# Kernel tuning notes

Hardware: AMD Instinct MI355X
Metric: run time of the kernel (lower is better)

## Reference

```python
import jax, jax.numpy as jnp
import numpy as np
from jax import lax

N, G, L, D, E, STEPS = 65536, 128, 512, 128, 262144, 6
C = 2 * D  # concat dim (input_dim + output_dim)


def setup_inputs() -> dict:
    key = jax.random.key(0)
    ks = jax.random.split(key, 12)
    sD = 1.0 / float(np.sqrt(D))
    sC = 1.0 / float(np.sqrt(C))
    return {
        "x": jax.random.normal(ks[0], (N, D), jnp.float32),
        "edge_index": jax.random.randint(ks[1], (2, E), 0, N, dtype=jnp.int32),
        "edge_weight": jax.random.uniform(ks[2], (E,), jnp.float32),
        "batch": (jnp.arange(N) // L).astype(jnp.int32),  # sorted graph ids, L nodes/graph
        "ggnn_w": jax.random.normal(ks[3], (STEPS, D, D), jnp.float32) * sD,
        "gru_wih": jax.random.normal(ks[4], (3 * D, D), jnp.float32) * sD,
        "gru_whh": jax.random.normal(ks[5], (3 * D, D), jnp.float32) * sD,
        "gru_bih": jnp.zeros((3 * D,), jnp.float32),
        "gru_bhh": jnp.zeros((3 * D,), jnp.float32),
        "conv1_w": jax.random.normal(ks[6], (D, D, 3), jnp.float32) * sD,
        "conv1_b": jnp.zeros((D,), jnp.float32),
        "conv2_w": jax.random.normal(ks[7], (D, D, 1), jnp.float32) * sD,
        "conv2_b": jnp.zeros((D,), jnp.float32),
        "convc1_w": jax.random.normal(ks[8], (C, C, 3), jnp.float32) * sC,
        "convc1_b": jnp.zeros((C,), jnp.float32),
        "convc2_w": jax.random.normal(ks[9], (C, C, 1), jnp.float32) * sC,
        "convc2_b": jnp.zeros((C,), jnp.float32),
        "bn1_g": jnp.ones((D,), jnp.float32),
        "bn1_b": jnp.zeros((D,), jnp.float32),
        "bn2_g": jnp.ones((C,), jnp.float32),
        "bn2_b": jnp.zeros((C,), jnp.float32),
        "mlpy_w": jax.random.normal(ks[10], (2, D), jnp.float32) * sD,
        "mlpy_b": jnp.zeros((2,), jnp.float32),
        "mlpz_w": jax.random.normal(ks[11], (2, C), jnp.float32) * sC,
        "mlpz_b": jnp.zeros((2,), jnp.float32),
    }


def _gru(m, h, wih, whh, bih, bhh):
    gx = m @ wih.T + bih
    gh = h @ whh.T + bhh
    xr, xz, xn = jnp.split(gx, 3, axis=-1)
    hr, hz, hn = jnp.split(gh, 3, axis=-1)
    r = jax.nn.sigmoid(xr + hr)
    z = jax.nn.sigmoid(xz + hz)
    n = jnp.tanh(xn + r * hn)
    return (1.0 - z) * n + z * h


def _conv1d(x, w, b):  # x [G,Cin,L], w [Cout,Cin,K]
    y = lax.conv_general_dilated(x, w, (1,), "VALID", dimension_numbers=("NCH", "OIH", "NCH"))
    return y + b[None, :, None]


def _maxpool(x, k, s):
    return lax.reduce_window(x, -jnp.inf, lax.max, (1, 1, k), (1, 1, s), "VALID")


def _bn(x, g, b):  # training-mode BatchNorm1d over (N, L) per channel
    mean = x.mean(axis=(0, 2), keepdims=True)
    var = x.var(axis=(0, 2), keepdims=True)
    return (x - mean) * lax.rsqrt(var + 1e-5) * g[None, :, None] + b[None, :, None]


def reference(x, edge_index, edge_weight, batch, ggnn_w, gru_wih, gru_whh, gru_bih,
              gru_bhh, conv1_w, conv1_b, conv2_w, conv2_b, convc1_w, convc1_b,
              convc2_w, convc2_b, bn1_g, bn1_b, bn2_g, bn2_b, mlpy_w, mlpy_b,
              mlpz_w, mlpz_b):
    src, dst = edge_index[0], edge_index[1]

    # GatedGraphConv: per layer linear -> weighted message scatter-add -> GRU update
    def step(h, w):
        m = h @ w
        agg = jax.ops.segment_sum(m[src] * edge_weight[:, None], dst, num_segments=N)
        return _gru(agg, h, gru_wih, gru_whh, gru_bih, gru_bhh), None

    h, _ = lax.scan(step, x, ggnn_w)

    # de_batchify_graphs: one fused scatter into zero-padded [G, L, *] tensor
    counts = jax.ops.segment_sum(jnp.ones((N,), jnp.int32), batch, num_segments=G)
    offsets = jnp.cumsum(counts) - counts
    pos = jnp.arange(N) - offsets[batch]
    x_i = jnp.zeros((G, L, D), x.dtype).at[batch, pos].set(x)
    h_i = jnp.zeros((G, L, D), h.dtype).at[batch, pos].set(h)
    c_i = jnp.concatenate([h_i, x_i], axis=-1)  # [G, L, 2D]

    hT = h_i.transpose(0, 2, 1)  # [G, D, L]
    Y1 = _maxpool(jax.nn.relu(_bn(_conv1d(hT, conv1_w, conv1_b), bn1_g, bn1_b)), 3, 2)
    Y2 = _maxpool(jax.nn.relu(_bn(_conv1d(Y1, conv2_w, conv2_b), bn1_g, bn1_b)), 2, 2).transpose(0, 2, 1)
    cT = c_i.transpose(0, 2, 1)  # [G, 2D, L]
    Z1 = _maxpool(jax.nn.relu(_bn(_conv1d(cT, convc1_w, convc1_b), bn2_g, bn2_b)), 3, 2)
    Z2 = _maxpool(jax.nn.relu(_bn(_conv1d(Z1, convc2_w, convc2_b), bn2_g, bn2_b)), 2, 2).transpose(0, 2, 1)

    before_avg = (Y2 @ mlpy_w.T + mlpy_b) * (Z2 @ mlpz_w.T + mlpz_b)  # [G, L', 2]
    return before_avg.mean(axis=1)  # [G, 2]
```

## Files before the change

### kernel.cpp

```cpp
#include <hip/hip_runtime.h>
#include <math.h>

#define NN 65536
#define GG 128
#define LL 512
#define DD 128
#define EE 262144
#define NSTEPS 6
#define CC 256
#define L1 510
#define P1 254
#define P2 127

typedef __attribute__((ext_vector_type(8))) short s8bf;
typedef __attribute__((ext_vector_type(4))) float f4acc;

__device__ __forceinline__ unsigned short f2bf(float x) {
  unsigned u = __float_as_uint(x);
  unsigned r = u + 0x7FFFu + ((u >> 16) & 1u);
  return (unsigned short)(r >> 16);
}
__device__ __forceinline__ float bf2f(unsigned short h) {
  return __uint_as_float(((unsigned)h) << 16);
}
__device__ __forceinline__ unsigned short f2bf_sel(float x, int lo_sel) {
  unsigned short hi = f2bf(x);
  if (!lo_sel) return hi;
  return f2bf(x - bf2f(hi));
}
__device__ __forceinline__ uint2 pack4bf(float4 v, int lo_sel) {
  unsigned short s0 = f2bf_sel(v.x, lo_sel), s1 = f2bf_sel(v.y, lo_sel);
  unsigned short s2 = f2bf_sel(v.z, lo_sel), s3 = f2bf_sel(v.w, lo_sel);
  uint2 pk; pk.x = (unsigned)s0 | ((unsigned)s1 << 16);
  pk.y = (unsigned)s2 | ((unsigned)s3 << 16);
  return pk;
}

__global__ __launch_bounds__(256) void k_prep(
    const float* __restrict__ wih, const float* __restrict__ whh,
    const float* __restrict__ gw,
    const float* __restrict__ w1, const float* __restrict__ wc1,
    const float* __restrict__ w2, const float* __restrict__ wc2,
    unsigned short* __restrict__ whhCh, unsigned short* __restrict__ whhCl,
    unsigned short* __restrict__ c1h, unsigned short* __restrict__ c1l,
    unsigned short* __restrict__ cc1h, unsigned short* __restrict__ cc1l,
    unsigned short* __restrict__ c2h, unsigned short* __restrict__ c2l,
    unsigned short* __restrict__ cc2h, unsigned short* __restrict__ cc2l) {
  int i = blockIdx.x * 256 + threadIdx.x;
  if (i < 49152) {
    float u = whh[i];
    unsigned short h2 = f2bf(u);
    whhCh[i] = h2; whhCl[i] = f2bf(u - bf2f(h2));
  }
  if (i < 49152) {
    int ci = i & 127; int r = i >> 7; int co = r & 127; int tap = r >> 7;
    float v = w1[(co * 128 + ci) * 3 + tap];
    unsigned short h_ = f2bf(v);
    c1h[i] = h_; c1l[i] = f2bf(v - bf2f(h_));
  }
  if (i < 196608) {
    int ci = i & 255; int r = i >> 8; int co = r & 255; int tap = r >> 8;
    float v = wc1[(co * 256 + ci) * 3 + tap];
    unsigned short h_ = f2bf(v);
    cc1h[i] = h_; cc1l[i] = f2bf(v - bf2f(h_));
  }
  if (i < 16384) {
    float v = w2[i];
    unsigned short h_ = f2bf(v);
    c2h[i] = h_; c2l[i] = f2bf(v - bf2f(h_));
  }
  if (i < 65536) {
    float v = wc2[i];
    unsigned short h_ = f2bf(v);
    cc2h[i] = h_; cc2l[i] = f2bf(v - bf2f(h_));
  }
}

__global__ __launch_bounds__(256) void k_combine(
    const float* __restrict__ gw, const float* __restrict__ wih,
    unsigned short* __restrict__ WcH, unsigned short* __restrict__ WcL) {
  int i = blockIdx.x * 256 + threadIdx.x;
  int s = i / 49152;
  int r = i % 49152;
  int d = r >> 7, k = r & 127;
  const float4* ga = (const float4*)&gw[(s << 14) + k * 128];
  const float4* wa = (const float4*)&wih[d * 128];
  float4 av = make_float4(0.f, 0.f, 0.f, 0.f);
#pragma unroll 8
  for (int c = 0; c < 32; c++) {
    float4 g4 = ga[c], w4 = wa[c];
    av.x += g4.x * w4.x; av.y += g4.y * w4.y;
    av.z += g4.z * w4.z; av.w += g4.w * w4.w;
  }
  float acc = (av.x + av.y) + (av.z + av.w);
  unsigned short h_ = f2bf(acc);
  WcH[i] = h_;
  WcL[i] = f2bf(acc - bf2f(h_));
}

__global__ __launch_bounds__(256) void k_castx(const float* __restrict__ x,
                                               unsigned short* __restrict__ xH,
                                               unsigned short* __restrict__ xL) {
  int i = blockIdx.x * 256 + threadIdx.x;
  const float4* x4 = (const float4*)x;
  float4 a = x4[i * 2 + 0];
  float4 b = x4[i * 2 + 1];
  uint2 ha = pack4bf(a, 0), hb = pack4bf(b, 0);
  uint2 la = pack4bf(a, 1), lb = pack4bf(b, 1);
  uint4 hv; hv.x = ha.x; hv.y = ha.y; hv.z = hb.x; hv.w = hb.y;
  uint4 lv; lv.x = la.x; lv.y = la.y; lv.z = lb.x; lv.w = lb.y;
  *(uint4*)&xH[i * 8] = hv;
  *(uint4*)&xL[i * 8] = lv;
}

__global__ __launch_bounds__(256) void k_hist(const int* __restrict__ dst, int* __restrict__ cnt) {
  int e = blockIdx.x * 256 + threadIdx.x;
  if (e < EE) atomicAdd(&cnt[dst[e]], 1);
}

__global__ __launch_bounds__(1024) void k_scan(const int* __restrict__ cnt,
                                               int* __restrict__ rowptr,
                                               int* __restrict__ cursor) {
  __shared__ int part[1024];
  int t = threadIdx.x;
  int base = t * 64;
  int s = 0;
  for (int i = 0; i < 64; i++) s += cnt[base + i];
  part[t] = s;
  __syncthreads();
  for (int off = 1; off < 1024; off <<= 1) {
    int v = part[t];
    int u = (t >= off) ? part[t - off] : 0;
    __syncthreads();
    part[t] = v + u;
    __syncthreads();
  }
  int run = part[t] - s;
  for (int i = 0; i < 64; i++) {
    rowptr[base + i] = run;
    cursor[base + i] = run;
    run += cnt[base + i];
  }
  if (t == 1023) rowptr[NN] = run;
}

__global__ __launch_bounds__(256) void k_fill(const int* __restrict__ src,
                                              const int* __restrict__ dst,
                                              const float* __restrict__ ew,
                                              int* __restrict__ cursor,
                                              int* __restrict__ col,
                                              float* __restrict__ wgt) {
  int e = blockIdx.x * 256 + threadIdx.x;
  if (e < EE) {
    int d = dst[e];
    int p = atomicAdd(&cursor[d], 1);
    col[p] = src[e];
    wgt[p] = ew[e];
  }
}

__global__ __launch_bounds__(256) void k_gather(
    const unsigned short* __restrict__ hH, const unsigned short* __restrict__ hL,
    const int* __restrict__ rowptr, const int* __restrict__ col,
    const float* __restrict__ wgt,
    unsigned short* __restrict__ aggH, unsigned short* __restrict__ aggL) {
  int t = threadIdx.x;
  int n = blockIdx.x * 8 + (t >> 5);
  int cb = (t & 31) * 4;
  int s0 = rowptr[n], s1 = rowptr[n + 1];
  float ax = 0.f, ay = 0.f, az = 0.f, aw = 0.f;
  int e = s0;
  for (; e + 2 <= s1; e += 2) {
    int cA = col[e], cB = col[e + 1];
    float wA = wgt[e], wB = wgt[e + 1];
    uint2 hA = *(const uint2*)&hH[cA * 128 + cb];
    uint2 lA = *(const uint2*)&hL[cA * 128 + cb];
    uint2 hB = *(const uint2*)&hH[cB * 128 + cb];
    uint2 lB = *(const uint2*)&hL[cB * 128 + cb];
    float a0 = __uint_as_float(hA.x << 16) + __uint_as_float(lA.x << 16);
    float a1 = __uint_as_float(hA.x & 0xFFFF0000u) + __uint_as_float(lA.x & 0xFFFF0000u);
    float a2 = __uint_as_float(hA.y << 16) + __uint_as_float(lA.y << 16);
    float a3 = __uint_as_float(hA.y & 0xFFFF0000u) + __uint_as_float(lA.y & 0xFFFF0000u);
    float b0 = __uint_as_float(hB.x << 16) + __uint_as_float(lB.x << 16);
    float b1 = __uint_as_float(hB.x & 0xFFFF0000u) + __uint_as_float(lB.x & 0xFFFF0000u);
    float b2 = __uint_as_float(hB.y << 16) + __uint_as_float(lB.y << 16);
    float b3 = __uint_as_float(hB.y & 0xFFFF0000u) + __uint_as_float(lB.y & 0xFFFF0000u);
    ax += a0 * wA + b0 * wB;
    ay += a1 * wA + b1 * wB;
    az += a2 * wA + b2 * wB;
    aw += a3 * wA + b3 * wB;
  }
  if (e < s1) {
    int cA = col[e];
    float wA = wgt[e];
    uint2 hA = *(const uint2*)&hH[cA * 128 + cb];
    uint2 lA = *(const uint2*)&hL[cA * 128 + cb];
    float a0 = __uint_as_float(hA.x << 16) + __uint_as_float(lA.x << 16);
    float a1 = __uint_as_float(hA.x & 0xFFFF0000u) + __uint_as_float(lA.x & 0xFFFF0000u);
    float a2 = __uint_as_float(hA.y << 16) + __uint_as_float(lA.y << 16);
    float a3 = __uint_as_float(hA.y & 0xFFFF0000u) + __uint_as_float(lA.y & 0xFFFF0000u);
    ax += a0 * wA; ay += a1 * wA; az += a2 * wA; aw += a3 * wA;
  }
  unsigned short h0 = f2bf(ax), h1 = f2bf(ay), h2 = f2bf(az), h3 = f2bf(aw);
  unsigned short l0 = f2bf(ax - bf2f(h0)), l1 = f2bf(ay - bf2f(h1));
  unsigned short l2 = f2bf(az - bf2f(h2)), l3 = f2bf(aw - bf2f(h3));
  uint2 hpk, lpk;
  hpk.x = (unsigned)h0 | ((unsigned)h1 << 16); hpk.y = (unsigned)h2 | ((unsigned)h3 << 16);
  lpk.x = (unsigned)l0 | ((unsigned)l1 << 16); lpk.y = (unsigned)l2 | ((unsigned)l3 << 16);
  int base = n * 128 + cb;
  *(uint2*)&aggH[base] = hpk;
  *(uint2*)&aggL[base] = lpk;
}

__global__ __launch_bounds__(256, 2) void k_gru_mfma(
    const unsigned short* __restrict__ aggH, const unsigned short* __restrict__ aggL,
    const unsigned short* __restrict__ hinH, const unsigned short* __restrict__ hinL,
    const unsigned short* __restrict__ wxh, const unsigned short* __restrict__ wxl,
    const unsigned short* __restrict__ whhCh, const unsigned short* __restrict__ whhCl,
    const float* __restrict__ bih, const float* __restrict__ bhh,
    unsigned short* __restrict__ houtH, unsigned short* __restrict__ houtL) {
  __shared__ __attribute__((aligned(16))) unsigned short As[2 * 64 * 136];
  int t = threadIdx.x;
  int r0 = blockIdx.x * 64;
  int d0 = blockIdx.y * 64;
  int wv = t >> 6, lane = t & 63;
  int ln = lane & 15, q = lane >> 4;
  f4acc acc[4][6];
#pragma unroll
  for (int mt = 0; mt < 4; mt++)
#pragma unroll
    for (int tg = 0; tg < 6; tg++) acc[mt][tg] = (f4acc)0.f;

  for (int p = 0; p < 3; p++) {
    if (p != 1) {
      const unsigned short* s0 = (p == 2) ? aggL : aggH;
      const unsigned short* s1 = (p == 2) ? hinL : hinH;
      if (p) __syncthreads();
#pragma unroll
      for (int it = 0; it < 8; it++) {
        int v8 = it * 256 + t;
        int mat = v8 >> 10;
        int row = (v8 >> 4) & 63, k = (v8 & 15) * 8;
        const unsigned short* S = mat ? s1 : s0;
        *(uint4*)&As[mat * 8704 + row * 136 + k] = *(const uint4*)&S[(r0 + row) * 128 + k];
      }
      __syncthreads();
    }
    const unsigned short* wx = (p == 1) ? wxl : wxh;
    const unsigned short* wh = (p == 1) ? whhCl : whhCh;
#pragma unroll
    for (int k0 = 0; k0 < 128; k0 += 32) {
      s8bf af[2][4], bfr[6];
#pragma unroll
      for (int tg = 0; tg < 6; tg++) {
        int gate = (tg < 3) ? tg : tg - 3;
        const unsigned short* W = (tg < 3) ? wx : wh;
        bfr[tg] = *(const s8bf*)&W[(gate * 128 + d0 + wv * 16 + ln) * 128 + k0 + q * 8];
      }
#pragma unroll
      for (int mat = 0; mat < 2; mat++)
#pragma unroll
        for (int mt = 0; mt < 4; mt++)
          af[mat][mt] = *(const s8bf*)&As[mat * 8704 + (mt * 16 + ln) * 136 + k0 + q * 8];
#pragma unroll
      for (int mt = 0; mt < 4; mt++)
#pragma unroll
        for (int tg = 0; tg < 6; tg++)
          acc[mt][tg] = __builtin_amdgcn_mfma_f32_16x16x32_bf16(
              af[tg < 3 ? 0 : 1][mt], bfr[tg], acc[mt][tg], 0, 0, 0);
    }
  }
  int d = d0 + wv * 16 + ln;
  float bi0 = bih[d], bi1 = bih[128 + d], bi2 = bih[256 + d];
  float bh0 = bhh[d], bh1 = bhh[128 + d], bh2 = bhh[256 + d];
#pragma unroll
  for (int mt = 0; mt < 4; mt++) {
#pragma unroll
    for (int reg = 0; reg < 4; reg++) {
      int r = r0 + mt * 16 + q * 4 + reg;
      int idx = r * 128 + d;
      float hold = bf2f(hinH[idx]) + bf2f(hinL[idx]);
      float xr = acc[mt][0][reg] + bi0;
      float xz = acc[mt][1][reg] + bi1;
      float xn = acc[mt][2][reg] + bi2;
      float hr = acc[mt][3][reg] + bh0;
      float hz = acc[mt][4][reg] + bh1;
      float hn = acc[mt][5][reg] + bh2;
      float rr = 1.f / (1.f + expf(-(xr + hr)));
      float zz = 1.f / (1.f + expf(-(xz + hz)));
      float nnv = tanhf(xn + rr * hn);
      float hv = (1.f - zz) * nnv + zz * hold;
      unsigned short hh = f2bf(hv);
      houtH[idx] = hh;
      houtL[idx] = f2bf(hv - bf2f(hh));
    }
  }
}

template<int CIN, int TAPS, int WA>
__global__ __launch_bounds__(256, 4) void k_conv_mfma(
    const unsigned short* __restrict__ hiA, const unsigned short* __restrict__ hiB,
    const unsigned short* __restrict__ loA, const unsigned short* __restrict__ loB,
    const unsigned short* __restrict__ Wh, const unsigned short* __restrict__ Wl,
    const float* __restrict__ bias, float* __restrict__ out,
    float* __restrict__ stats, int Lin, int Lco) {
  constexpr int APAD = CIN + 8;
  constexpr int ROWS = 64 + TAPS - 1;
  constexpr int NCH = CIN / 32;
  constexpr int TOT8 = ROWS * CIN / 8;
  constexpr int NIT = (TOT8 + 255) / 256;
  constexpr int NINNER = TAPS * NCH;
  __shared__ __attribute__((aligned(16))) unsigned short As[ROWS * APAD];
  __shared__ float sred[256];
  const int g = blockIdx.z, co0 = blockIdx.y * 128, l0 = blockIdx.x * 64;
  const int t = threadIdx.x;
  const int wv = t >> 6, lane = t & 63, ln = lane & 15, q = lane >> 4;
  f4acc acc[4][2];
#pragma unroll
  for (int mt = 0; mt < 4; mt++)
#pragma unroll
    for (int nt = 0; nt < 2; nt++) acc[mt][nt] = (f4acc)0.f;

  for (int p = 0; p < 3; p++) {
    if (p != 1) {
      const unsigned short* pA = (p == 2) ? loA : hiA;
      const unsigned short* pB = (p == 2) ? loB : hiB;
      if (p) __syncthreads();
#pragma unroll
      for (int it = 0; it < NIT; it++) {
        int v8 = it * 256 + t;
        if (NIT * 256 == TOT8 || v8 < TOT8) {
          int row = (v8 * 8) / CIN, ch = (v8 * 8) % CIN;
          int lr = l0 + row; if (lr > Lin - 1) lr = Lin - 1;
          uint4 v;
          if (ch < WA) v = *(const uint4*)&pA[(g * Lin + lr) * WA + ch];
          else         v = *(const uint4*)&pB[(g * Lin + lr) * WA + ch - WA];
          *(uint4*)&As[row * APAD + ch] = v;
        }
      }
      __syncthreads();
    }
    const unsigned short* W = (p == 1) ? Wl : Wh;
    s8bf bcur[2], bnxt[2];
#pragma unroll
    for (int nt = 0; nt < 2; nt++)
      bcur[nt] = *(const s8bf*)&W[(co0 + wv * 32 + nt * 16 + ln) * CIN + q * 8];
#pragma unroll
    for (int it = 0; it < NINNER; it++) {
      const int tap = it / NCH, ch = it % NCH;
      if (it + 1 < NINNER) {
        const int ntap = (it + 1) / NCH, nch = (it + 1) % NCH;
#pragma unroll
        for (int nt = 0; nt < 2; nt++)
          bnxt[nt] = *(const s8bf*)&W[(ntap * CIN + co0 + wv * 32 + nt * 16 + ln) * CIN + nch * 32 + q * 8];
      }
      const int c0 = ch * 32;
      s8bf af[4];
#pragma unroll
      for (int mt = 0; mt < 4; mt++)
        af[mt] = *(const s8bf*)&As[(mt * 16 + ln + tap) * APAD + c0 + q * 8];
#pragma unroll
      for (int mt = 0; mt < 4; mt++)
#pragma unroll
        for (int nt = 0; nt < 2; nt++)
          acc[mt][nt] = __builtin_amdgcn_mfma_f32_16x16x32_bf16(af[mt], bcur[nt], acc[mt][nt], 0, 0, 0);
      if (it + 1 < NINNER) { bcur[0] = bnxt[0]; bcur[1] = bnxt[1]; }
    }
  }
  sred[t] = 0.f;
  __syncthreads();
#pragma unroll
  for (int nt = 0; nt < 2; nt++) {
    int cl = wv * 32 + nt * 16 + ln;
    int co = co0 + cl;
    float bv = bias[co];
    float s = 0.f, s2 = 0.f;
#pragma unroll
    for (int mt = 0; mt < 4; mt++)
#pragma unroll
      for (int reg = 0; reg < 4; reg++) {
        int l = l0 + mt * 16 + q * 4 + reg;
        if (l < Lco) {
          float v = acc[mt][nt][reg] + bv;
          out[(g * Lco + l) * CIN + co] = v;
          s += v; s2 += v * v;
        }
      }
    atomicAdd(&sred[cl], s);
    atomicAdd(&sred[128 + cl], s2);
  }
  __syncthreads();
  if (t < 128) atomicAdd(&stats[co0 + t], sred[t]);
  else atomicAdd(&stats[CIN + co0 + (t - 128)], sred[t]);
}

template<bool PLANES>
__global__ __launch_bounds__(256) void k_bnpool(const float* __restrict__ in,
                                                float* __restrict__ outF,
                                                unsigned short* __restrict__ outH,
                                                unsigned short* __restrict__ outL,
                                                const float* __restrict__ stats,
                                                const float* __restrict__ gamma,
                                                const float* __restrict__ beta,
                                                int Cch, int LinC, int Lout, int pk) {
  int idx = blockIdx.x * 256 + threadIdx.x;
  int total = GG * Cch * Lout;
  if (idx >= total) return;
  int c = idx & (Cch - 1);
  int r = idx / Cch;
  int p = r % Lout;
  int g = r / Lout;
  float cntf = (float)(GG * LinC);
  float mean = stats[c] / cntf;
  float var = stats[Cch + c] / cntf - mean * mean;
  float inv = rsqrtf(var + 1e-5f) * gamma[c];
  float sh = beta[c] - mean * inv;
  const float* base = &in[((g * LinC) + 2 * p) * Cch + c];
  float m = 0.f;
  for (int k = 0; k < pk; k++) {
    float v = fmaxf(base[k * Cch] * inv + sh, 0.f);
    m = fmaxf(m, v);
  }
  int o = (g * Lout + p) * Cch + c;
  if (PLANES) {
    unsigned short hh = f2bf(m);
    outH[o] = hh;
    outL[o] = f2bf(m - bf2f(hh));
  } else {
    outF[o] = m;
  }
}

__global__ __launch_bounds__(128) void k_final(const float* __restrict__ Y2,
                                               const float* __restrict__ Z2,
                                               const float* __restrict__ myw,
                                               const float* __restrict__ myb,
                                               const float* __restrict__ mzw,
                                               const float* __restrict__ mzb,
                                               float* __restrict__ outp) {
  __shared__ float red0[128];
  __shared__ float red1[128];
  int g = blockIdx.x;
  int t = threadIdx.x;
  float y0 = myb[0], y1 = myb[1], z0 = mzb[0], z1 = mzb[1];
  if (t < P2) {
    const float* yb = &Y2[(g * P2 + t) * 128];
    for (int c = 0; c < 128; c++) {
      float v = yb[c];
      y0 += v * myw[c];
      y1 += v * myw[128 + c];
    }
    const float* zb = &Z2[(g * P2 + t) * 256];
    for (int c = 0; c < 256; c++) {
      float v = zb[c];
      z0 += v * mzw[c];
      z1 += v * mzw[256 + c];
    }
  }
  red0[t] = (t < P2) ? y0 * z0 : 0.f;
  red1[t] = (t < P2) ? y1 * z1 : 0.f;
  __syncthreads();
  for (int off = 64; off > 0; off >>= 1) {
    if (t < off) {
      red0[t] += red0[t + off];
      red1[t] += red1[t + off];
    }
    __syncthreads();
  }
  if (t == 0) {
    outp[g * 2 + 0] = red0[0] / 127.f;
    outp[g * 2 + 1] = red1[0] / 127.f;
  }
}

extern "C" void kernel_launch(void* const* d_in, const int* in_sizes, int n_in,
                              void* d_out, int out_size, void* d_ws, size_t ws_size,
                              hipStream_t stream) {
  const float* x   = (const float*)d_in[0];
  const int* ei    = (const int*)d_in[1];
  const float* ew  = (const float*)d_in[2];
  const float* gw  = (const float*)d_in[4];
  const float* wih = (const float*)d_in[5];
  const float* whh = (const float*)d_in[6];
  const float* bih = (const float*)d_in[7];
  const float* bhh = (const float*)d_in[8];
  const float* w1  = (const float*)d_in[9];
  const float* b1  = (const float*)d_in[10];
  const float* w2  = (const float*)d_in[11];
  const float* b2  = (const float*)d_in[12];
  const float* wc1 = (const float*)d_in[13];
  const float* bc1 = (const float*)d_in[14];
  const float* wc2 = (const float*)d_in[15];
  const float* bc2 = (const float*)d_in[16];
  const float* bn1g = (const float*)d_in[17];
  const float* bn1b = (const float*)d_in[18];
  const float* bn2g = (const float*)d_in[19];
  const float* bn2b = (const float*)d_in[20];
  const float* myw = (const float*)d_in[21];
  const float* myb = (const float*)d_in[22];
  const float* mzw = (const float*)d_in[23];
  const float* mzb = (const float*)d_in[24];
  float* out = (float*)d_out;

  float* ws = (float*)d_ws;
  unsigned short* PH = (unsigned short*)ws;
  unsigned short* PL = PH + 8388608;
  unsigned short* xH = PL + 8388608;
  unsigned short* xL = xH + 8388608;
  unsigned short* c1h  = xL + 8388608;
  unsigned short* c1l  = c1h + 49152;
  unsigned short* cc1h = c1l + 49152;
  unsigned short* cc1l = cc1h + 196608;
  unsigned short* c2h  = cc1l + 196608;
  unsigned short* c2l  = c2h + 16384;
  unsigned short* cc2h = c2l + 16384;
  unsigned short* cc2l = cc2h + 65536;
  float* stats = (float*)(cc2l + 65536);
  float* Y2 = stats + 512;
  float* Z2 = Y2 + 2080768;
  float* shared0 = Z2 + 4161536;
  unsigned short* QH = (unsigned short*)shared0;
  unsigned short* QL = QH + 8388608;
  unsigned short* WcCh = QL + 8388608;
  unsigned short* WcCl = WcCh + 294912;
  unsigned short* aggH = WcCl + 294912;
  unsigned short* aggL = aggH + 8388608;
  unsigned short* whhCh = aggL + 8388608;
  unsigned short* whhCl = whhCh + 49152;
  int* cnt    = (int*)(whhCl + 49152);
  int* rowptr = cnt + 65536;
  int* cursor = rowptr + 65537;
  int* col    = cursor + 65536;
  float* wgt  = (float*)(col + 262144);
  float* ggnn_end = wgt + 262144;
  float* bufA = shared0;
  unsigned short* bufBH = (unsigned short*)(bufA + 16711680);
  unsigned short* bufBL = bufBH + 8323072;
  float* conv_end = (float*)(bufBL + 8323072);
  float* wend = (ggnn_end > conv_end) ? ggnn_end : conv_end;
  size_t needed = (size_t)(wend - ws) * 4;
  if (ws_size < needed) return;

  const int* src = ei;
  const int* dst = ei + EE;

  k_prep<<<768, 256, 0, stream>>>(wih, whh, gw, w1, wc1, w2, wc2,
                                  whhCh, whhCl,
                                  c1h, c1l, cc1h, cc1l, c2h, c2l, cc2h, cc2l);
  k_combine<<<1152, 256, 0, stream>>>(gw, wih, WcCh, WcCl);
  k_castx<<<4096, 256, 0, stream>>>(x, xH, xL);
  hipMemsetAsync(cnt, 0, 65536 * 4, stream);
  k_hist<<<1024, 256, 0, stream>>>(dst, cnt);
  k_scan<<<1, 1024, 0, stream>>>(cnt, rowptr, cursor);
  k_fill<<<1024, 256, 0, stream>>>(src, dst, ew, cursor, col, wgt);

  for (int s = 0; s < NSTEPS; s++) {
    const unsigned short* AH = (s == 0) ? xH : ((s & 1) ? QH : PH);
    const unsigned short* AL = (s == 0) ? xL : ((s & 1) ? QL : PL);
    unsigned short* OH = (s & 1) ? PH : QH;
    unsigned short* OL = (s & 1) ? PL : QL;
    k_gather<<<8192, 256, 0, stream>>>(AH, AL, rowptr, col, wgt, aggH, aggL);
    k_gru_mfma<<<dim3(1024, 2), 256, 0, stream>>>(aggH, aggL, AH, AL,
                                                  WcCh + s * 49152, WcCl + s * 49152,
                                                  whhCh, whhCl, bih, bhh, OH, OL);
  }

  hipMemsetAsync(stats, 0, 512 * 4, stream);
  k_conv_mfma<128, 3, 128><<<dim3(8, 1, 128), 256, 0, stream>>>(
      PH, nullptr, PL, nullptr, c1h, c1l, b1, bufA, stats, 512, L1);
  k_bnpool<true><<<(GG * 128 * P1 + 255) / 256, 256, 0, stream>>>(
      bufA, nullptr, bufBH, bufBL, stats, bn1g, bn1b, 128, L1, P1, 3);
  hipMemsetAsync(stats, 0, 512 * 4, stream);
  k_conv_mfma<128, 1, 128><<<dim3(4, 1, 128), 256, 0, stream>>>(
      bufBH, nullptr, bufBL, nullptr, c2h, c2l, b2, bufA, stats, P1, P1);
  k_bnpool<false><<<(GG * 128 * P2 + 255) / 256, 256, 0, stream>>>(
      bufA, Y2, nullptr, nullptr, stats, bn1g, bn1b, 128, P1, P2, 2);

  hipMemsetAsync(stats, 0, 512 * 4, stream);
  k_conv_mfma<256, 3, 128><<<dim3(8, 2, 128), 256, 0, stream>>>(
      PH, xH, PL, xL, cc1h, cc1l, bc1, bufA, stats, 512, L1);
  k_bnpool<true><<<(GG * 256 * P1 + 255) / 256, 256, 0, stream>>>(
      bufA, nullptr, bufBH, bufBL, stats, bn2g, bn2b, 256, L1, P1, 3);
  hipMemsetAsync(stats, 0, 512 * 4, stream);
  k_conv_mfma<256, 1, 256><<<dim3(4, 2, 128), 256, 0, stream>>>(
      bufBH, nullptr, bufBL, nullptr, cc2h, cc2l, bc2, bufA, stats, P1, P1);
  k_bnpool<false><<<(GG * 256 * P2 + 255) / 256, 256, 0, stream>>>(
      bufA, Z2, nullptr, nullptr, stats, bn2g, bn2b, 256, P1, P2, 2);

  k_final<<<128, 128, 0, stream>>>(Y2, Z2, myw, myb, mzw, mzb, out);
}
```

Baseline: 1.471 ms.

## Vectorize BN-pool and final reduction, unroll gather loop by four

Three changes land together. The edge gather loop is unrolled from two to four edges per iteration to expose more independent loads. The BN+ReLU+maxpool kernel now handles four channels per thread with float4 loads and packed bf16 stores. The final MLP/mean kernel uses wave-level shuffle reductions over coalesced rows instead of one thread walking a whole row. Together these aim to cut memory-latency stalls and uncoalesced access in the smaller post-GGNN kernels, at the cost of relying on a pack4bf helper and on channel counts divisible by four.

Result: no change. 1.448 ms (median of 2 runs) (-1.6%).

```diff
diff --git a/kernel.cpp b/kernel.cpp
--- a/kernel.cpp
+++ b/kernel.cpp
@@ -159,6 +159,19 @@
   }
 }
 
+__device__ __forceinline__ void acc_edge(const unsigned short* __restrict__ hH,
+                                         const unsigned short* __restrict__ hL,
+                                         int cA, int cb, float wA,
+                                         float& ax, float& ay, float& az, float& aw) {
+  uint2 h_ = *(const uint2*)&hH[cA * 128 + cb];
+  uint2 l_ = *(const uint2*)&hL[cA * 128 + cb];
+  float a0 = __uint_as_float(h_.x << 16) + __uint_as_float(l_.x << 16);
+  float a1 = __uint_as_float(h_.x & 0xFFFF0000u) + __uint_as_float(l_.x & 0xFFFF0000u);
+  float a2 = __uint_as_float(h_.y << 16) + __uint_as_float(l_.y << 16);
+  float a3 = __uint_as_float(h_.y & 0xFFFF0000u) + __uint_as_float(l_.y & 0xFFFF0000u);
+  ax += a0 * wA; ay += a1 * wA; az += a2 * wA; aw += a3 * wA;
+}
+
 __global__ __launch_bounds__(256) void k_gather(
     const unsigned short* __restrict__ hH, const unsigned short* __restrict__ hL,
     const int* __restrict__ rowptr, const int* __restrict__ col,
@@ -170,36 +183,16 @@
   int s0 = rowptr[n], s1 = rowptr[n + 1];
   float ax = 0.f, ay = 0.f, az = 0.f, aw = 0.f;
   int e = s0;
-  for (; e + 2 <= s1; e += 2) {
-    int cA = col[e], cB = col[e + 1];
-    float wA = wgt[e], wB = wgt[e + 1];
-    uint2 hA = *(const uint2*)&hH[cA * 128 + cb];
-    uint2 lA = *(const uint2*)&hL[cA * 128 + cb];
-    uint2 hB = *(const uint2*)&hH[cB * 128 + cb];
-    uint2 lB = *(const uint2*)&hL[cB * 128 + cb];
-    float a0 = __uint_as_float(hA.x << 16) + __uint_as_float(lA.x << 16);
-    float a1 = __uint_as_float(hA.x & 0xFFFF0000u) + __uint_as_float(lA.x & 0xFFFF0000u);
-    float a2 = __uint_as_float(hA.y << 16) + __uint_as_float(lA.y << 16);
-    float a3 = __uint_as_float(hA.y & 0xFFFF0000u) + __uint_as_float(lA.y & 0xFFFF0000u);
-    float b0 = __uint_as_float(hB.x << 16) + __uint_as_float(lB.x << 16);
-    float b1 = __uint_as_float(hB.x & 0xFFFF0000u) + __uint_as_float(lB.x & 0xFFFF0000u);
-    float b2 = __uint_as_float(hB.y << 16) + __uint_as_float(lB.y << 16);
-    float b3 = __uint_as_float(hB.y & 0xFFFF0000u) + __uint_as_float(lB.y & 0xFFFF0000u);
-    ax += a0 * wA + b0 * wB;
-    ay += a1 * wA + b1 * wB;
-    az += a2 * wA + b2 * wB;
-    aw += a3 * wA + b3 * wB;
-  }
-  if (e < s1) {
-    int cA = col[e];
-    float wA = wgt[e];
-    uint2 hA = *(const uint2*)&hH[cA * 128 + cb];
-    uint2 lA = *(const uint2*)&hL[cA * 128 + cb];
-    float a0 = __uint_as_float(hA.x << 16) + __uint_as_float(lA.x << 16);
-    float a1 = __uint_as_float(hA.x & 0xFFFF0000u) + __uint_as_float(lA.x & 0xFFFF0000u);
-    float a2 = __uint_as_float(hA.y << 16) + __uint_as_float(lA.y << 16);
-    float a3 = __uint_as_float(hA.y & 0xFFFF0000u) + __uint_as_float(lA.y & 0xFFFF0000u);
-    ax += a0 * wA; ay += a1 * wA; az += a2 * wA; aw += a3 * wA;
+  for (; e + 4 <= s1; e += 4) {
+    int cA = col[e], cB = col[e + 1], cC = col[e + 2], cD = col[e + 3];
+    float wA = wgt[e], wB = wgt[e + 1], wC = wgt[e + 2], wD = wgt[e + 3];
+    acc_edge(hH, hL, cA, cb, wA, ax, ay, az, aw);
+    acc_edge(hH, hL, cB, cb, wB, ax, ay, az, aw);
+    acc_edge(hH, hL, cC, cb, wC, ax, ay, az, aw);
+    acc_edge(hH, hL, cD, cb, wD, ax, ay, az, aw);
+  }
+  for (; e < s1; e++) {
+    acc_edge(hH, hL, col[e], cb, wgt[e], ax, ay, az, aw);
   }
   unsigned short h0 = f2bf(ax), h1 = f2bf(ay), h2 = f2bf(az), h3 = f2bf(aw);
   unsigned short l0 = f2bf(ax - bf2f(h0)), l1 = f2bf(ay - bf2f(h1));
@@ -404,72 +397,86 @@
                                                 const float* __restrict__ beta,
                                                 int Cch, int LinC, int Lout, int pk) {
   int idx = blockIdx.x * 256 + threadIdx.x;
-  int total = GG * Cch * Lout;
+  int c4n = Cch >> 2;
+  int total = GG * c4n * Lout;
   if (idx >= total) return;
-  int c = idx & (Cch - 1);
-  int r = idx / Cch;
+  int c = (idx % c4n) * 4;
+  int r = idx / c4n;
   int p = r % Lout;
   int g = r / Lout;
   float cntf = (float)(GG * LinC);
-  float mean = stats[c] / cntf;
-  float var = stats[Cch + c] / cntf - mean * mean;
-  float inv = rsqrtf(var + 1e-5f) * gamma[c];
-  float sh = beta[c] - mean * inv;
+  float4 st0 = *(const float4*)&stats[c];
+  float4 st1 = *(const float4*)&stats[Cch + c];
+  float4 gm = *(const float4*)&gamma[c];
+  float4 bt = *(const float4*)&beta[c];
+  float4 inv, sh;
+  {
+    float m0 = st0.x / cntf, m1 = st0.y / cntf, m2 = st0.z / cntf, m3 = st0.w / cntf;
+    inv.x = rsqrtf(st1.x / cntf - m0 * m0 + 1e-5f) * gm.x;
+    inv.y = rsqrtf(st1.y / cntf - m1 * m1 + 1e-5f) * gm.y;
+    inv.z = rsqrtf(st1.z / cntf - m2 * m2 + 1e-5f) * gm.z;
+    inv.w = rsqrtf(st1.w / cntf - m3 * m3 + 1e-5f) * gm.w;
+    sh.x = bt.x - m0 * inv.x; sh.y = bt.y - m1 * inv.y;
+    sh.z = bt.z - m2 * inv.z; sh.w = bt.w - m3 * inv.w;
+  }
   const float* base = &in[((g * LinC) + 2 * p) * Cch + c];
-  float m = 0.f;
+  float4 m = make_float4(0.f, 0.f, 0.f, 0.f);
   for (int k = 0; k < pk; k++) {
-    float v = fmaxf(base[k * Cch] * inv + sh, 0.f);
-    m = fmaxf(m, v);
+    float4 v = *(const float4*)&base[k * Cch];
+    m.x = fmaxf(m.x, fmaxf(v.x * inv.x + sh.x, 0.f));
+    m.y = fmaxf(m.y, fmaxf(v.y * inv.y + sh.y, 0.f));
+    m.z = fmaxf(m.z, fmaxf(v.z * inv.z + sh.z, 0.f));
+    m.w = fmaxf(m.w, fmaxf(v.w * inv.w + sh.w, 0.f));
   }
   int o = (g * Lout + p) * Cch + c;
   if (PLANES) {
-    unsigned short hh = f2bf(m);
-    outH[o] = hh;
-    outL[o] = f2bf(m - bf2f(hh));
+    *(uint2*)&outH[o] = pack4bf(m, 0);
+    *(uint2*)&outL[o] = pack4bf(m, 1);
   } else {
-    outF[o] = m;
-  }
-}
-
-__global__ __launch_bounds__(128) void k_final(const float* __restrict__ Y2,
+    *(float4*)&outF[o] = m;
+  }
+}
+
+__global__ __launch_bounds__(256) void k_final(const float* __restrict__ Y2,
                                                const float* __restrict__ Z2,
                                                const float* __restrict__ myw,
                                                const float* __restrict__ myb,
                                                const float* __restrict__ mzw,
                                                const float* __restrict__ mzb,
                                                float* __restrict__ outp) {
-  __shared__ float red0[128];
-  __shared__ float red1[128];
+  __shared__ float red0[4];
+  __shared__ float red1[4];
   int g = blockIdx.x;
   int t = threadIdx.x;
-  float y0 = myb[0], y1 = myb[1], z0 = mzb[0], z1 = mzb[1];
-  if (t < P2) {
-    const float* yb = &Y2[(g * P2 + t) * 128];
-    for (int c = 0; c < 128; c++) {
-      float v = yb[c];
-      y0 += v * myw[c];
-      y1 += v * myw[128 + c];
+  int wv = t >> 6, lane = t & 63;
+  float2 wy0 = *(const float2*)&myw[lane * 2];
+  float2 wy1 = *(const float2*)&myw[128 + lane * 2];
+  float4 wz0 = *(const float4*)&mzw[lane * 4];
+  float4 wz1 = *(const float4*)&mzw[256 + lane * 4];
+  float yb0 = myb[0], yb1 = myb[1], zb0 = mzb[0], zb1 = mzb[1];
+  float acc0 = 0.f, acc1 = 0.f;
+  for (int l = wv; l < P2; l += 4) {
+    float2 yv = *(const float2*)&Y2[(g * P2 + l) * 128 + lane * 2];
+    float4 zv = *(const float4*)&Z2[(g * P2 + l) * 256 + lane * 4];
+    float y0 = yv.x * wy0.x + yv.y * wy0.y;
+    float y1 = yv.x * wy1.x + yv.y * wy1.y;
+    float z0 = zv.x * wz0.x + zv.y * wz0.y + zv.z * wz0.z + zv.w * wz0.w;
+    float z1 = zv.x * wz1.x + zv.y * wz1.y + zv.z * wz1.z + zv.w * wz1.w;
+#pragma unroll
+    for (int off = 32; off > 0; off >>= 1) {
+      y0 += __shfl_xor(y0, off);
+      y1 += __shfl_xor(y1, off);
+      z0 += __shfl_xor(z0, off);
+      z1 += __shfl_xor(z1, off);
     }
-    const float* zb = &Z2[(g * P2 + t) * 256];
-    for (int c = 0; c < 256; c++) {
-      float v = zb[c];
-      z0 += v * mzw[c];
-      z1 += v * mzw[256 + c];
-    }
-  }
-  red0[t] = (t < P2) ? y0 * z0 : 0.f;
-  red1[t] = (t < P2) ? y1 * z1 : 0.f;
+    acc0 += (y0 + yb0) * (z0 + zb0);
+    acc1 += (y1 + yb1) * (z1 + zb1);
+  }
+  if (lane == 0) { red0[wv] = acc0; red1[wv] = acc1; }
   __syncthreads();
-  for (int off = 64; off > 0; off >>= 1) {
-    if (t < off) {
-      red0[t] += red0[t + off];
-      red1[t] += red1[t + off];
-    }
-    __syncthreads();
-  }
   if (t == 0) {
-    outp[g * 2 + 0] = red0[0] / 127.f;
-    outp[g * 2 + 1] = red1[0] / 127.f;
+    outp[g * 2 + 0] = (red0[0] + red0[1] + red0[2] + red0[3]) / 127.f;
+    outp[g * 2 + 1] = (red1[0] + red1[1] + red1[2] + red1[3]) / 127.f;
   }
 }
 
@@ -568,24 +575,24 @@
   hipMemsetAsync(stats, 0, 512 * 4, stream);
   k_conv_mfma<128, 3, 128><<<dim3(8, 1, 128), 256, 0, stream>>>(
       PH, nullptr, PL, nullptr, c1h, c1l, b1, bufA, stats, 512, L1);
-  k_bnpool<true><<<(GG * 128 * P1 + 255) / 256, 256, 0, stream>>>(
+  k_bnpool<true><<<(GG * 128 * P1 / 4 + 255) / 256, 256, 0, stream>>>(
       bufA, nullptr, bufBH, bufBL, stats, bn1g, bn1b, 128, L1, P1, 3);
   hipMemsetAsync(stats, 0, 512 * 4, stream);
   k_conv_mfma<128, 1, 128><<<dim3(4, 1, 128), 256, 0, stream>>>(
       bufBH, nullptr, bufBL, nullptr, c2h, c2l, b2, bufA, stats, P1, P1);
-  k_bnpool<false><<<(GG * 128 * P2 + 255) / 256, 256, 0, stream>>>(
+  k_bnpool<false><<<(GG * 128 * P2 / 4 + 255) / 256, 256, 0, stream>>>(
       bufA, Y2, nullptr, nullptr, stats, bn1g, bn1b, 128, P1, P2, 2);
 
   hipMemsetAsync(stats, 0, 512 * 4, stream);
   k_conv_mfma<256, 3, 128><<<dim3(8, 2, 128), 256, 0, stream>>>(
       PH, xH, PL, xL, cc1h, cc1l, bc1, bufA, stats, 512, L1);
-  k_bnpool<true><<<(GG * 256 * P1 + 255) / 256, 256, 0, stream>>>(
+  k_bnpool<true><<<(GG * 256 * P1 / 4 + 255) / 256, 256, 0, stream>>>(
       bufA, nullptr, bufBH, bufBL, stats, bn2g, bn2b, 256, L1, P1, 3);
   hipMemsetAsync(stats, 0, 512 * 4, stream);
   k_conv_mfma<256, 1, 256><<<dim3(4, 2, 128), 256, 0, stream>>>(
       bufBH, nullptr, bufBL, nullptr, cc2h, cc2l, bc2, bufA, stats, P1, P1);
-  k_bnpool<false><<<(GG * 256 * P2 + 255) / 256, 256, 0, stream>>>(
+  k_bnpool<false><<<(GG * 256 * P2 / 4 + 255) / 256, 256, 0, stream>>>(
       bufA, Z2, nullptr, nullptr, stats, bn2g, bn2b, 256, P1, P2, 2);
 
-  k_final<<<128, 128, 0, stream>>>(Y2, Z2, myw, myb, mzw, mzb, out);
-}
+  k_final<<<128, 256, 0, stream>>>(Y2, Z2, myw, myb, mzw, mzb, out);
+}
```
